# Kernel tuning notes

Measured on AMD Instinct MI355X. Metric: run time of the kernel, lower is better.

## Reference

```python
import jax, jax.numpy as jnp
import numpy as np

FEATURE_DIM = 2048
EMBED_DIM = 512
HIDDEN_DIM = 512
VOCAB_SIZE = 10000
ATT_DIM = 512
BATCH = 32
NUM_PIXELS = 196
MAX_LEN = 20


def setup_inputs() -> dict:
    key = jax.random.key(0)
    ks = jax.random.split(key, 16)
    def p(k, shape, scale=0.02):
        return jax.random.normal(k, shape, dtype=jnp.float32) * scale
    return {
        "features": jax.random.normal(ks[0], (BATCH, NUM_PIXELS, FEATURE_DIM), dtype=jnp.float32),
        "captions": jax.random.randint(ks[1], (BATCH, MAX_LEN), 0, VOCAB_SIZE),
        "emb": p(ks[2], (VOCAB_SIZE, EMBED_DIM)),
        "W_ih": p(ks[3], (4 * HIDDEN_DIM, EMBED_DIM + FEATURE_DIM)),
        "b_ih": jnp.zeros((4 * HIDDEN_DIM,), dtype=jnp.float32),
        "W_hh": p(ks[4], (4 * HIDDEN_DIM, HIDDEN_DIM)),
        "b_hh": jnp.zeros((4 * HIDDEN_DIM,), dtype=jnp.float32),
        "fc_W": p(ks[5], (VOCAB_SIZE, HIDDEN_DIM)),
        "fc_b": jnp.zeros((VOCAB_SIZE,), dtype=jnp.float32),
        "enc_W": p(ks[6], (ATT_DIM, FEATURE_DIM)),
        "enc_b": jnp.zeros((ATT_DIM,), dtype=jnp.float32),
        "dec_W": p(ks[7], (ATT_DIM, HIDDEN_DIM)),
        "dec_b": jnp.zeros((ATT_DIM,), dtype=jnp.float32),
        "full_W": p(ks[8], (1, ATT_DIM)),
        "full_b": jnp.zeros((1,), dtype=jnp.float32),
    }


def reference(features, captions, emb, W_ih, b_ih, W_hh, b_hh, fc_W, fc_b,
              enc_W, enc_b, dec_W, dec_b, full_W, full_b):
    # embeddings: [B, T, E] -> scan over time as [T, B, E]
    embeddings = emb[captions]
    xs = jnp.swapaxes(embeddings, 0, 1)
    B = features.shape[0]
    h0 = jnp.zeros((B, HIDDEN_DIM), dtype=features.dtype)
    c0 = jnp.zeros((B, HIDDEN_DIM), dtype=features.dtype)
    # encoder projection of features is time-invariant: [B, P, A]
    enc_proj = jnp.einsum('bpf,af->bpa', features, enc_W) + enc_b

    def step(carry, x_t):
        h, c = carry
        # Bahdanau attention
        dec_proj = h @ dec_W.T + dec_b                      # [B, A]
        e = jnp.einsum('bpa,a->bp', jax.nn.relu(enc_proj + dec_proj[:, None, :]), full_W[0]) + full_b[0]
        alpha = jax.nn.softmax(e, axis=1)                   # [B, P]
        context = jnp.einsum('bp,bpf->bf', alpha, features) # [B, F]
        # LSTMCell
        lstm_in = jnp.concatenate([x_t, context], axis=1)
        gates = lstm_in @ W_ih.T + b_ih + h @ W_hh.T + b_hh
        i, f, g, o = jnp.split(gates, 4, axis=1)
        i = jax.nn.sigmoid(i)
        f = jax.nn.sigmoid(f)
        g = jnp.tanh(g)
        o = jax.nn.sigmoid(o)
        c_new = f * c + i * g
        h_new = o * jnp.tanh(c_new)
        # dropout in eval mode = identity
        out = h_new @ fc_W.T + fc_b                         # [B, V]
        return (h_new, c_new), out

    _, outs = jax.lax.scan(step, (h0, c0), xs)
    return jnp.swapaxes(outs, 0, 1)  # [B, T, V]
```

## Files before the change

### kernel.cpp

```cpp
#include <hip/hip_runtime.h>
#include <math.h>

#define B_   32
#define P_   196
#define F_   2048
#define E_   512
#define H_   512
#define V_   10000
#define T_   20
#define GSZ  8
#define NBLK (B_ * GSZ)

typedef unsigned short ushort_t;
typedef ushort_t u16x8 __attribute__((ext_vector_type(8)));
typedef ushort_t u16x2 __attribute__((ext_vector_type(2)));
typedef short    bf16x8 __attribute__((ext_vector_type(8)));
typedef float    f32x4  __attribute__((ext_vector_type(4)));

__device__ __forceinline__ ushort_t bf_rne(float x) {
    union { float f; unsigned u; } v; v.f = x;
    unsigned r = v.u + 0x7FFFu + ((v.u >> 16) & 1u);
    return (ushort_t)(r >> 16);
}
__device__ __forceinline__ float b2f(ushort_t u) {
    union { unsigned u; float f; } v; v.u = ((unsigned)u) << 16;
    return v.f;
}

__device__ __forceinline__ int permc(int chunk) {
    int gi = chunk >> 6, r = chunk & 63;
    return (r & 7) * 32 + (r >> 3) * 4 + gi;
}

__global__ __launch_bounds__(256)
void cvt_all_kernel(const float* __restrict__ feat, const float* __restrict__ enc_W,
                    const float* __restrict__ fc_W, const float* __restrict__ dec_W,
                    const float* __restrict__ W_ih, const float* __restrict__ W_hh,
                    const float* __restrict__ emb, const int* __restrict__ captions,
                    const float* __restrict__ b_ih, const float* __restrict__ b_hh,
                    ushort_t* __restrict__ featB, ushort_t* __restrict__ encWB,
                    ushort_t* __restrict__ fcWB, ushort_t* __restrict__ decWB,
                    ushort_t* __restrict__ WihCB, ushort_t* __restrict__ WihEB,
                    ushort_t* __restrict__ WhhT, ushort_t* __restrict__ XB,
                    float* __restrict__ bsum, float* __restrict__ zbuf)
{
    const int blk = blockIdx.x, tid = threadIdx.x;
    if (blk < 6272) {
        size_t i = (size_t)blk * 2048 + tid * 8;
        float4 a = *(const float4*)&feat[i], b = *(const float4*)&feat[i + 4];
        u16x8 o; o[0]=bf_rne(a.x); o[1]=bf_rne(a.y); o[2]=bf_rne(a.z); o[3]=bf_rne(a.w);
        o[4]=bf_rne(b.x); o[5]=bf_rne(b.y); o[6]=bf_rne(b.z); o[7]=bf_rne(b.w);
        *(u16x8*)&featB[i] = o;
    } else if (blk < 6784) {
        size_t i = (size_t)(blk - 6272) * 2048 + tid * 8;
        float4 a = *(const float4*)&enc_W[i], b = *(const float4*)&enc_W[i + 4];
        u16x8 o; o[0]=bf_rne(a.x); o[1]=bf_rne(a.y); o[2]=bf_rne(a.z); o[3]=bf_rne(a.w);
        o[4]=bf_rne(b.x); o[5]=bf_rne(b.y); o[6]=bf_rne(b.z); o[7]=bf_rne(b.w);
        *(u16x8*)&encWB[i] = o;
    } else if (blk < 9284) {
        size_t i = (size_t)(blk - 6784) * 2048 + tid * 8;
        float4 a = *(const float4*)&fc_W[i], b = *(const float4*)&fc_W[i + 4];
        u16x8 o; o[0]=bf_rne(a.x); o[1]=bf_rne(a.y); o[2]=bf_rne(a.z); o[3]=bf_rne(a.w);
        o[4]=bf_rne(b.x); o[5]=bf_rne(b.y); o[6]=bf_rne(b.z); o[7]=bf_rne(b.w);
        *(u16x8*)&fcWB[i] = o;
    } else if (blk < 9412) {
        size_t i = (size_t)(blk - 9284) * 2048 + tid * 8;
        float4 a = *(const float4*)&dec_W[i], b = *(const float4*)&dec_W[i + 4];
        u16x8 o; o[0]=bf_rne(a.x); o[1]=bf_rne(a.y); o[2]=bf_rne(a.z); o[3]=bf_rne(a.w);
        o[4]=bf_rne(b.x); o[5]=bf_rne(b.y); o[6]=bf_rne(b.z); o[7]=bf_rne(b.w);
        *(u16x8*)&decWB[i] = o;
    } else if (blk < 11460) {
        int j = blk - 9412, f = tid * 8;
        int Pj = permc(j >> 3) * 8 + (j & 7);
        const float* s = &W_ih[(size_t)j * 2560 + 512 + f];
        float4 a = *(const float4*)&s[0], b = *(const float4*)&s[4];
        u16x8 o; o[0]=bf_rne(a.x); o[1]=bf_rne(a.y); o[2]=bf_rne(a.z); o[3]=bf_rne(a.w);
        o[4]=bf_rne(b.x); o[5]=bf_rne(b.y); o[6]=bf_rne(b.z); o[7]=bf_rne(b.w);
        *(u16x8*)&WihCB[(size_t)Pj * 2048 + f] = o;
    } else if (blk < 11972) {
        size_t idx = (size_t)(blk - 11460) * 2048 + tid * 8;
        int j = (int)(idx >> 9), f = (int)(idx & 511);
        int Pj = permc(j >> 3) * 8 + (j & 7);
        const float* s = &W_ih[(size_t)j * 2560 + f];
        float4 a = *(const float4*)&s[0], b = *(const float4*)&s[4];
        u16x8 o; o[0]=bf_rne(a.x); o[1]=bf_rne(a.y); o[2]=bf_rne(a.z); o[3]=bf_rne(a.w);
        o[4]=bf_rne(b.x); o[5]=bf_rne(b.y); o[6]=bf_rne(b.z); o[7]=bf_rne(b.w);
        *(u16x8*)&WihEB[(size_t)Pj * 512 + f] = o;
    } else if (blk < 12484) {
        int k = blk - 11972, j0 = tid * 8;
        int nc = permc(tid);
        u16x8 o;
#pragma unroll
        for (int q = 0; q < 8; q++) o[q] = bf_rne(W_hh[(size_t)(j0 + q) * 512 + k]);
        *(u16x8*)&WhhT[(size_t)k * 2048 + nc * 8] = o;
    } else if (blk < 13124) {
        int m = blk - 12484;
        int tt = m >> 5, b = m & 31;
        int cap = captions[b * T_ + tt];
        int i = tid * 2;
        u16x2 o;
        o[0] = bf_rne(emb[(size_t)cap * 512 + i]);
        o[1] = bf_rne(emb[(size_t)cap * 512 + i + 1]);
        *(u16x2*)&XB[(size_t)m * 512 + i] = o;
    } else {
        int nc = permc(tid);
        int j0 = tid * 8;
#pragma unroll
        for (int q = 0; q < 8; q++) {
            bsum[nc * 8 + q] = b_ih[j0 + q] + b_hh[j0 + q];
            zbuf[j0 + q] = 0.f;
        }
    }
}

__global__ __launch_bounds__(256)
void mfma_gemm_kernel(const ushort_t* __restrict__ A, const ushort_t* __restrict__ B,
                      const float* __restrict__ bias, ushort_t* __restrict__ Cb,
                      float* __restrict__ Cf, int K, int N, int mode)
{
    __shared__ ushort_t As[128][32];
    __shared__ ushort_t Bs[128][32];
    const int tid = threadIdx.x;
    const int m0 = blockIdx.x * 128, n0 = blockIdx.y * 128;
    const int wave = tid >> 6, lane = tid & 63;
    const int wm = (wave & 1) * 64, wn = (wave >> 1) * 64;
    const int lm = lane & 15, lk = (lane >> 4) * 8;

    f32x4 acc[4][4];
#pragma unroll
    for (int mt = 0; mt < 4; mt++)
#pragma unroll
        for (int nt = 0; nt < 4; nt++)
#pragma unroll
            for (int r = 0; r < 4; r++) acc[mt][nt][r] = 0.f;

    for (int k0 = 0; k0 < K; k0 += 32) {
#pragma unroll
        for (int i = 0; i < 2; i++) {
            int gi  = tid + i * 256;
            int row = gi >> 2;
            int gr  = (gi & 3) * 8;
            *(u16x8*)&As[row][gr] = *(const u16x8*)&A[(size_t)(m0 + row) * K + k0 + gr];
            int brow = n0 + row; if (brow >= N) brow = N - 1;
            *(u16x8*)&Bs[row][gr] = *(const u16x8*)&B[(size_t)brow * K + k0 + gr];
        }
        __syncthreads();
        bf16x8 af[4], bv[4];
#pragma unroll
        for (int mt = 0; mt < 4; mt++)
            af[mt] = *(const bf16x8*)&As[wm + mt * 16 + lm][lk];
#pragma unroll
        for (int nt = 0; nt < 4; nt++)
            bv[nt] = *(const bf16x8*)&Bs[wn + nt * 16 + lm][lk];
#pragma unroll
        for (int mt = 0; mt < 4; mt++)
#pragma unroll
            for (int nt = 0; nt < 4; nt++)
                acc[mt][nt] = __builtin_amdgcn_mfma_f32_16x16x32_bf16(
                    af[mt], bv[nt], acc[mt][nt], 0, 0, 0);
        __syncthreads();
    }

    const int rb = (lane >> 4) * 4;
#pragma unroll
    for (int nt = 0; nt < 4; nt++) {
        int n = n0 + wn + nt * 16 + lm;
        int nc = n < N ? n : N - 1;
        float bz = (mode == 3) ? 0.f : bias[nc];
#pragma unroll
        for (int mt = 0; mt < 4; mt++) {
            int mbase = m0 + wm + mt * 16 + rb;
#pragma unroll
            for (int r = 0; r < 4; r++) {
                int m = mbase + r;
                float v = acc[mt][nt][r] + ((mode == 3) ? bias[m] : bz);
                if (mode == 0 || mode == 3) {
                    Cb[(size_t)m * N + n] = bf_rne(v);
                } else if (n < N) {
                    int crow = (mode == 1) ? ((m & 31) * 20 + (m >> 5)) : m;
                    Cf[(size_t)crow * N + n] = v;
                }
            }
        }
    }
}

__device__ __forceinline__ void wait_cnt(unsigned* p, unsigned target) {
    if (threadIdx.x == 0) {
        while (__hip_atomic_load(p, __ATOMIC_RELAXED, __HIP_MEMORY_SCOPE_AGENT) < target)
            __builtin_amdgcn_s_sleep(1);
    }
    __syncthreads();
}

__global__ __launch_bounds__(256, 1)
void persist_kernel(float* __restrict__ hbuf,
                    ushort_t* __restrict__ hseqB,
                    const ushort_t* __restrict__ encPT,
                    const ushort_t* __restrict__ decWB,
                    const float* __restrict__ dec_b,
                    const float* __restrict__ full_W,
                    const float* __restrict__ full_b,
                    const ushort_t* __restrict__ GB,
                    const ushort_t* __restrict__ WhhT,
                    const float* __restrict__ xproj,
                    float* __restrict__ epartG,
                    unsigned* __restrict__ hcnt,
                    unsigned* __restrict__ ecnt)
{
    __shared__ ushort_t Gs[196][256];
    __shared__ float hsh[512];
    __shared__ float fws[512];
    __shared__ float dps64[64];
    __shared__ float es[200];
    __shared__ float al[200];
    __shared__ float sred[8][32][9];
    __shared__ float gsh[256];

    const int tid = threadIdx.x;
    const int b = blockIdx.x & 31;
    const int s = blockIdx.x >> 5;
    unsigned* hcn = &hcnt[b * 32];
    unsigned* ecn = &ecnt[b * 32];
    float* epb = epartG + (size_t)b * 1600;

    {
        const int r0 = tid >> 5, c = (tid & 31) * 8;
        for (int i = 0; i < 25; i++) {
            int r = i * 8 + r0;
            if (r < 196)
                *(u16x8*)&Gs[r][c] =
                    *(const u16x8*)&GB[((size_t)(b * P_ + r)) * 2048 + s * 256 + c];
        }
    }
    if (tid < 128)
        *(float4*)&fws[tid * 4] = *(const float4*)&full_W[tid * 4];

    const int lane = tid & 63, wave = tid >> 6;
    const int g16 = lane >> 4, gl = lane & 15;
    const int kg = tid >> 5, cg = tid & 31;
    const float fb0 = full_b[0];
    float c_reg = 0.f;

    for (int t = 0; t < T_; t++) {
        if (t == 0) {
            hsh[tid * 2] = 0.f; hsh[tid * 2 + 1] = 0.f;
        } else {
            wait_cnt(hcn, 8u * (unsigned)t);
            const float* hb = hbuf + ((size_t)(t & 1) * 32 + b) * 512;
            hsh[tid * 2] = __hip_atomic_load(&hb[tid * 2],
                                             __ATOMIC_RELAXED, __HIP_MEMORY_SCOPE_AGENT);
            hsh[tid * 2 + 1] = __hip_atomic_load(&hb[tid * 2 + 1],
                                             __ATOMIC_RELAXED, __HIP_MEMORY_SCOPE_AGENT);
        }
        __syncthreads();

        if (t == 0) {
            if (tid < 64) dps64[tid] = dec_b[s * 64 + tid];
        } else {
#pragma unroll
            for (int q = 0; q < 4; q++) {
                int a = wave * 16 + q * 4 + g16;
                const ushort_t* wr = decWB + (size_t)(s * 64 + a) * 512;
                float sacc = 0.f;
#pragma unroll
                for (int jj = 0; jj < 4; jj++) {
                    u16x8 wv = *(const u16x8*)&wr[jj * 128 + gl * 8];
                    float4 h0 = *(float4*)&hsh[jj * 128 + gl * 8];
                    float4 h1 = *(float4*)&hsh[jj * 128 + gl * 8 + 4];
                    sacc += b2f(wv[0]) * h0.x + b2f(wv[1]) * h0.y
                          + b2f(wv[2]) * h0.z + b2f(wv[3]) * h0.w
                          + b2f(wv[4]) * h1.x + b2f(wv[5]) * h1.y
                          + b2f(wv[6]) * h1.z + b2f(wv[7]) * h1.w;
                }
                sacc += __shfl_xor(sacc, 1, 64); sacc += __shfl_xor(sacc, 2, 64);
                sacc += __shfl_xor(sacc, 4, 64); sacc += __shfl_xor(sacc, 8, 64);
                if (gl == 0) dps64[a] = sacc + dec_b[s * 64 + a];
            }
        }
        __syncthreads();

        if (tid < 196) {
            const ushort_t* ep = encPT + (size_t)(s * 64) * 6272 + b * P_ + tid;
            float e = 0.f;
#pragma unroll 8
            for (int a = 0; a < 64; a++)
                e += fmaxf(b2f(ep[(size_t)a * 6272]) + dps64[a], 0.f) * fws[s * 64 + a];
            __hip_atomic_store(&epb[s * 200 + tid], e,
                               __ATOMIC_RELAXED, __HIP_MEMORY_SCOPE_AGENT);
        }
        __syncthreads();
        if (tid == 0)
            __hip_atomic_fetch_add(ecn, 1u,
                                   __ATOMIC_RELEASE, __HIP_MEMORY_SCOPE_AGENT);

        {
            float wa[8] = {0.f,0.f,0.f,0.f,0.f,0.f,0.f,0.f};
            const ushort_t* wp = WhhT + (size_t)(kg * 64) * 2048 + s * 256 + cg * 8;
#pragma unroll 8
            for (int kk = 0; kk < 64; kk++) {
                u16x8 wv = *(const u16x8*)&wp[(size_t)kk * 2048];
                float hv = hsh[kg * 64 + kk];
#pragma unroll
                for (int q = 0; q < 8; q++) wa[q] += b2f(wv[q]) * hv;
            }
#pragma unroll
            for (int q = 0; q < 8; q++) sred[kg][cg][q] = wa[q];
        }
        __syncthreads();
        float g = xproj[(size_t)(t * 32 + b) * 2048 + s * 256 + tid];
#pragma unroll
        for (int k2 = 0; k2 < 8; k2++) g += sred[k2][tid >> 3][tid & 7];

        wait_cnt(ecn, 8u * (unsigned)(t + 1));
        if (tid < 196) {
            float e = fb0;
#pragma unroll
            for (int s2 = 0; s2 < 8; s2++)
                e += __hip_atomic_load(&epb[s2 * 200 + tid],
                                       __ATOMIC_RELAXED, __HIP_MEMORY_SCOPE_AGENT);
            es[tid] = e;
        }
        __syncthreads();
        if (tid < 64) {
            float v[4]; int pv[4]; int n = 0;
            for (int q = 0; q < 4; q++) {
                int p = tid + 64 * q;
                if (p < P_) { pv[n] = p; v[n] = es[p]; n++; }
            }
            float m = -1e30f;
            for (int q = 0; q < n; q++) m = fmaxf(m, v[q]);
#pragma unroll
            for (int off = 32; off > 0; off >>= 1) m = fmaxf(m, __shfl_xor(m, off, 64));
            float ssum = 0.f;
            for (int q = 0; q < n; q++) { v[q] = expf(v[q] - m); ssum += v[q]; }
#pragma unroll
            for (int off = 32; off > 0; off >>= 1) ssum += __shfl_xor(ssum, off, 64);
            float rinv = 1.f / ssum;
            for (int q = 0; q < n; q++) al[pv[q]] = v[q] * rinv;
        }
        __syncthreads();

        {
            int p0 = (kg < 4) ? kg * 25 : 100 + (kg - 4) * 24;
            int np = (kg < 4) ? 25 : 24;
            float pa[8] = {0.f,0.f,0.f,0.f,0.f,0.f,0.f,0.f};
#pragma unroll 4
            for (int i = 0; i < np; i++) {
                int p = p0 + i;
                float av = al[p];
                u16x8 gv = *(const u16x8*)&Gs[p][cg * 8];
#pragma unroll
                for (int q = 0; q < 8; q++) pa[q] += b2f(gv[q]) * av;
            }
#pragma unroll
            for (int q = 0; q < 8; q++) sred[kg][cg][q] = pa[q];
        }
        __syncthreads();
#pragma unroll
        for (int k2 = 0; k2 < 8; k2++) g += sred[k2][tid >> 3][tid & 7];
        gsh[tid] = g;
        __syncthreads();

        if (tid < 64) {
            int ri = tid >> 3, e = tid & 7;
            float gi = gsh[ri * 32 + e];
            float gf = gsh[ri * 32 + 8 + e];
            float gg = gsh[ri * 32 + 16 + e];
            float go = gsh[ri * 32 + 24 + e];
            float ig = 1.f / (1.f + expf(-gi));
            float fg = 1.f / (1.f + expf(-gf));
            float g_ = tanhf(gg);
            float og = 1.f / (1.f + expf(-go));
            c_reg = fg * c_reg + ig * g_;
            float hn = og * tanhf(c_reg);
            int u = 8 * s + 64 * ri + e;
            float* ho = hbuf + ((size_t)((t + 1) & 1) * 32 + b) * 512 + u;
            __hip_atomic_store(ho, hn, __ATOMIC_RELAXED, __HIP_MEMORY_SCOPE_AGENT);
            hseqB[(size_t)(t + 1) * 16384 + b * 512 + u] = bf_rne(hn);
        }
        __syncthreads();
        if (tid == 0)
            __hip_atomic_fetch_add(hcn, 1u,
                                   __ATOMIC_RELEASE, __HIP_MEMORY_SCOPE_AGENT);
    }
}

extern "C" void kernel_launch(void* const* d_in, const int* in_sizes, int n_in,
                              void* d_out, int out_size, void* d_ws, size_t ws_size,
                              hipStream_t stream)
{
    (void)in_sizes; (void)n_in; (void)out_size; (void)ws_size;
    const float* feat   = (const float*)d_in[0];
    const int*   caps   = (const int*)  d_in[1];
    const float* emb    = (const float*)d_in[2];
    const float* W_ih   = (const float*)d_in[3];
    const float* b_ih   = (const float*)d_in[4];
    const float* W_hh   = (const float*)d_in[5];
    const float* b_hh   = (const float*)d_in[6];
    const float* fc_W   = (const float*)d_in[7];
    const float* fc_b   = (const float*)d_in[8];
    const float* enc_W  = (const float*)d_in[9];
    const float* enc_b  = (const float*)d_in[10];
    const float* dec_W  = (const float*)d_in[11];
    const float* dec_b  = (const float*)d_in[12];
    const float* full_W = (const float*)d_in[13];
    const float* full_b = (const float*)d_in[14];
    float* out = (float*)d_out;

    char* w = (char*)d_ws;
    ushort_t* featB = (ushort_t*)w;              w += 25690112;
    ushort_t* encWB = (ushort_t*)w;              w += 2097152;
    ushort_t* fcWB  = (ushort_t*)w;              w += 10240000;
    ushort_t* decWB = (ushort_t*)w;              w += 524288;
    ushort_t* WihCB = (ushort_t*)w;              w += 8388608;
    ushort_t* WihEB = (ushort_t*)w;              w += 2097152;
    ushort_t* WhhT  = (ushort_t*)w;              w += 2097152;
    ushort_t* XB    = (ushort_t*)w;              w += 655360;
    ushort_t* encPT = (ushort_t*)w;              w += 6422528;
    ushort_t* GB    = (ushort_t*)w;              w += 25690112;
    float*    xproj = (float*)w;                 w += 5242880;
    float*    bsum  = (float*)w;                 w += 8192;
    float*    zbuf  = (float*)w;                 w += 8192;
    float*    hbuf  = (float*)w;                 w += 131072;
    ushort_t* hseqB = (ushort_t*)w;              w += 688128;
    unsigned* hcnt  = (unsigned*)w;              w += 4096;
    unsigned* ecnt  = (unsigned*)w;              w += 4096;
    float*    epartG= (float*)w;                 w += 204800;

    hipMemsetAsync(hcnt, 0, 8192, stream);

    cvt_all_kernel<<<13125, 256, 0, stream>>>(
        feat, enc_W, fc_W, dec_W, W_ih, W_hh, emb, caps, b_ih, b_hh,
        featB, encWB, fcWB, decWB, WihCB, WihEB, WhhT, XB, bsum, zbuf);

    mfma_gemm_kernel<<<dim3(4, 49), 256, 0, stream>>>(
        encWB, featB, enc_b, encPT, nullptr, 2048, 6272, 3);

    mfma_gemm_kernel<<<dim3(49, 16), 256, 0, stream>>>(
        featB, WihCB, zbuf, GB, nullptr, 2048, 2048, 0);

    mfma_gemm_kernel<<<dim3(5, 16), 256, 0, stream>>>(
        XB, WihEB, bsum, nullptr, xproj, 512, 2048, 2);

    persist_kernel<<<NBLK, 256, 0, stream>>>(
        hbuf, hseqB, encPT, decWB, dec_b, full_W, full_b,
        GB, WhhT, xproj, epartG, hcnt, ecnt);

    mfma_gemm_kernel<<<dim3(5, 79), 256, 0, stream>>>(
        hseqB + 16384, fcWB, fc_b, nullptr, out, 512, V_, 1);
}
```

Before: 841.0 us.

## Cache recurrent weights in registers, encoder projection in LDS, and use direct-to-LDS loads

The persistent recurrent kernel now loads its W_hh slice into registers (64 vectors of 8 bf16 per thread) and its encoder-projection slice into shared memory once before the time loop. This removes repeated global or L2 reads on every one of the 20 serial steps. The GEMM tile loader switches to global_load_lds so data goes straight from global memory into LDS without passing through registers. The register cache needs about 256 VGPRs per thread and the extra LDS array pushes total shared memory near the per-block limit, which risks spilling or launch failure. The direct-to-LDS store layout also assumes a lane-ordered placement that has to match the original As/Bs indexing.

Result: slower. 877.9 us (+4.4%).

```diff
diff --git a/kernel.cpp b/kernel.cpp
--- a/kernel.cpp
+++ b/kernel.cpp
@@ -25,6 +25,12 @@
 __device__ __forceinline__ float b2f(ushort_t u) {
     union { unsigned u; float f; } v; v.u = ((unsigned)u) << 16;
     return v.f;
+}
+
+__device__ __forceinline__ void gl_lds16(const ushort_t* g, ushort_t* l) {
+    __builtin_amdgcn_global_load_lds(
+        (const __attribute__((address_space(1))) void*)g,
+        (__attribute__((address_space(3))) void*)l, 16, 0, 0);
 }
 
 __device__ __forceinline__ int permc(int chunk) {
@@ -140,9 +146,11 @@
             int gi  = tid + i * 256;
             int row = gi >> 2;
             int gr  = (gi & 3) * 8;
-            *(u16x8*)&As[row][gr] = *(const u16x8*)&A[(size_t)(m0 + row) * K + k0 + gr];
+            ushort_t* lbA = &As[0][0] + (size_t)(wave * 64 + i * 256) * 8;
+            ushort_t* lbB = &Bs[0][0] + (size_t)(wave * 64 + i * 256) * 8;
+            gl_lds16(&A[(size_t)(m0 + row) * K + k0 + gr], lbA);
             int brow = n0 + row; if (brow >= N) brow = N - 1;
-            *(u16x8*)&Bs[row][gr] = *(const u16x8*)&B[(size_t)brow * K + k0 + gr];
+            gl_lds16(&B[(size_t)brow * K + k0 + gr], lbB);
         }
         __syncthreads();
         bf16x8 af[4], bv[4];
@@ -209,6 +217,7 @@
                     unsigned* __restrict__ ecnt)
 {
     __shared__ ushort_t Gs[196][256];
+    __shared__ ushort_t ePs[64][200];
     __shared__ float hsh[512];
     __shared__ float fws[512];
     __shared__ float dps64[64];
@@ -233,6 +242,14 @@
                     *(const u16x8*)&GB[((size_t)(b * P_ + r)) * 2048 + s * 256 + c];
         }
     }
+    for (int it = 0; it < 25; it++) {
+        int idx = it * 256 + tid;
+        if (idx < 6272) {
+            int a = idx / 98, pp = idx - a * 98;
+            *(u16x2*)&ePs[a][pp * 2] =
+                *(const u16x2*)&encPT[(size_t)(s * 64 + a) * 6272 + b * P_ + pp * 2];
+        }
+    }
     if (tid < 128)
         *(float4*)&fws[tid * 4] = *(const float4*)&full_W[tid * 4];
 
@@ -241,6 +258,14 @@
     const int kg = tid >> 5, cg = tid & 31;
     const float fb0 = full_b[0];
     float c_reg = 0.f;
+
+    u16x8 wreg[64];
+    {
+        const ushort_t* wp0 = WhhT + (size_t)(kg * 64) * 2048 + s * 256 + cg * 8;
+#pragma unroll
+        for (int kk = 0; kk < 64; kk++)
+            wreg[kk] = *(const u16x8*)&wp0[(size_t)kk * 2048];
+    }
 
     for (int t = 0; t < T_; t++) {
         if (t == 0) {
@@ -281,11 +306,10 @@
         __syncthreads();
 
         if (tid < 196) {
-            const ushort_t* ep = encPT + (size_t)(s * 64) * 6272 + b * P_ + tid;
             float e = 0.f;
 #pragma unroll 8
             for (int a = 0; a < 64; a++)
-                e += fmaxf(b2f(ep[(size_t)a * 6272]) + dps64[a], 0.f) * fws[s * 64 + a];
+                e += fmaxf(b2f(ePs[a][tid]) + dps64[a], 0.f) * fws[s * 64 + a];
             __hip_atomic_store(&epb[s * 200 + tid], e,
                                __ATOMIC_RELAXED, __HIP_MEMORY_SCOPE_AGENT);
         }
@@ -296,10 +320,9 @@
 
         {
             float wa[8] = {0.f,0.f,0.f,0.f,0.f,0.f,0.f,0.f};
-            const ushort_t* wp = WhhT + (size_t)(kg * 64) * 2048 + s * 256 + cg * 8;
-#pragma unroll 8
+#pragma unroll
             for (int kk = 0; kk < 64; kk++) {
-                u16x8 wv = *(const u16x8*)&wp[(size_t)kk * 2048];
+                u16x8 wv = wreg[kk];
                 float hv = hsh[kg * 64 + kk];
 #pragma unroll
                 for (int q = 0; q < 8; q++) wa[q] += b2f(wv[q]) * hv;
```
